# Optimization experiments

Measured on AMD Instinct MI355X. Metric: run time of the kernel, lower is better.

## Reference

```python
import jax, jax.numpy as jnp
import numpy as np

B, N, FEAT, HID, H = 4, 2048, 512, 512, 8
HD = HID // H  # head_dim = 64


def rotate_half(x):
    # pairs along last dim: (x1, x2) -> (-x2, x1), interleaved
    x = x.reshape(*x.shape[:-1], -1, 2)
    x1, x2 = x[..., 0], x[..., 1]
    return jnp.stack((-x2, x1), axis=-1).reshape(*x.shape[:-2], -1)


def apply_rope(freqs, t):
    # freqs: [2, B, 1, N, HD] broadcasting over heads; t: [B, H, N, HD]
    return t * freqs[0] + rotate_half(t) * freqs[1]


def setup_inputs() -> dict:
    key = jax.random.key(0)
    ks = jax.random.split(key, 12)
    s = 0.02
    return {
        "x0": jax.random.normal(ks[0], (B, N, FEAT), jnp.float32),
        "x1": jax.random.normal(ks[1], (B, N, FEAT), jnp.float32),
        "encoding0": jax.random.normal(ks[2], (2, B, 1, N, HD), jnp.float32),
        "encoding1": jax.random.normal(ks[3], (2, B, 1, N, HD), jnp.float32),
        "Wqkv": jax.random.normal(ks[4], (FEAT, 3 * HID), jnp.float32) * s,
        "bqkv": jnp.zeros((3 * HID,), jnp.float32),
        "Wproj": jax.random.normal(ks[5], (HID, HID), jnp.float32) * s,
        "bproj": jnp.zeros((HID,), jnp.float32),
        "W1": jax.random.normal(ks[6], (FEAT + HID, 2 * FEAT), jnp.float32) * s,
        "b1": jnp.zeros((2 * FEAT,), jnp.float32),
        "ln_g": jnp.ones((2 * FEAT,), jnp.float32),
        "ln_b": jnp.zeros((2 * FEAT,), jnp.float32),
        "W2": jax.random.normal(ks[7], (2 * FEAT, FEAT), jnp.float32) * s,
        "b2": jnp.zeros((FEAT,), jnp.float32),
    }


def _block(x, enc, Wqkv, bqkv, Wproj, bproj, W1, b1, ln_g, ln_b, W2, b2):
    b, n, _ = x.shape
    qkv = x @ Wqkv + bqkv                                   # [B,N,3*HID]
    qkv = qkv.reshape(b, n, H, HD, 3).transpose(0, 2, 1, 3, 4)  # [B,H,N,HD,3]
    q, k, v = qkv[..., 0], qkv[..., 1], qkv[..., 2]
    q = apply_rope(enc, q)
    k = apply_rope(enc, k)
    scale = q.shape[-1] ** (-0.5)
    attn = jax.nn.softmax(jnp.einsum('bhid,bhjd->bhij', q, k) * scale, axis=-1)
    o = jnp.einsum('bhij,bhjd->bhid', attn, v)              # [B,H,N,HD]
    message = o.transpose(0, 2, 1, 3).reshape(b, n, HID) @ Wproj + bproj
    h = jnp.concatenate([x, message], axis=-1) @ W1 + b1    # [B,N,2*FEAT]
    mu = h.mean(-1, keepdims=True)
    var = ((h - mu) ** 2).mean(-1, keepdims=True)
    h = (h - mu) * jax.lax.rsqrt(var + 1e-5) * ln_g + ln_b
    return x + jax.nn.gelu(h, approximate=False) @ W2 + b2


def reference(x0, x1, encoding0, encoding1, Wqkv, bqkv, Wproj, bproj, W1, b1, ln_g, ln_b, W2, b2):
    p = (Wqkv, bqkv, Wproj, bproj, W1, b1, ln_g, ln_b, W2, b2)
    return (_block(x0, encoding0, *p), _block(x1, encoding1, *p))
```

## Files before the change

### kernel.cpp

```cpp
#include <hip/hip_runtime.h>
#include <hip/hip_bf16.h>

typedef __attribute__((ext_vector_type(8))) short   short8v;
typedef __attribute__((ext_vector_type(4))) short   short4v;
typedef __attribute__((ext_vector_type(8))) __bf16  bf16x8;
typedef __attribute__((ext_vector_type(4))) __bf16  bf16x4;
typedef __attribute__((ext_vector_type(4))) float   f32x4;

constexpr int Nn = 2048;

#define GLOAD_LDS(src, dst) \
  __builtin_amdgcn_global_load_lds((__attribute__((address_space(1))) unsigned int*)(src), \
                                   (__attribute__((address_space(3))) unsigned int*)(dst), 16, 0, 0)

#if __has_builtin(__builtin_amdgcn_exp2f)
#define EXP2F(x) __builtin_amdgcn_exp2f(x)
#else
#define EXP2F(x) exp2f(x)
#endif

#if __has_builtin(__builtin_amdgcn_mfma_f32_16x16x16bf16_1k)
#define HAVE_MFMA16 1
#define MFMA16(a, b, c) __builtin_amdgcn_mfma_f32_16x16x16bf16_1k(a, b, c, 0, 0, 0)
#else
#define HAVE_MFMA16 0
#endif

__device__ __forceinline__ unsigned pack_bf16(float lo, float hi) {
  union { __bf16 h[2]; unsigned u; } t;
  t.h[0] = (__bf16)lo; t.h[1] = (__bf16)hi;
  return t.u;
}

template<int AMODE, int BMODE, int EPI>
__global__ __launch_bounds__(256)
void gemm_mfma(const __bf16* __restrict__ A, const __bf16* __restrict__ A2,
               const __bf16* __restrict__ BT, const __bf16* __restrict__ BT2,
               const float* __restrict__ bias,
               const float* __restrict__ resid0, const float* __restrict__ resid1,
               float* __restrict__ Cf, __bf16* __restrict__ Cb, __bf16* __restrict__ Vt,
               int lda, int ldb, int ldb2, int ldc, int K1, int K)
{
  __shared__ __align__(16) __bf16 As[3][4096];
  __shared__ __align__(16) __bf16 Bs[3][4096];
  const int tid = threadIdx.x;
  const int w = tid >> 6, l = tid & 63;
  const int wr = w >> 1, wc = w & 1;
  const int lr = l & 15, lg = l >> 4;
  const int row0 = blockIdx.x * 128, col0 = blockIdx.y * 128;

  f32x4 acc[4][4];
#pragma unroll
  for (int i = 0; i < 4; ++i)
#pragma unroll
    for (int j = 0; j < 4; ++j) acc[i][j] = (f32x4){0.f, 0.f, 0.f, 0.f};

  const int srow = l >> 2;
  const int skk  = (l & 3) * 8;

  auto stage = [&](int k0, int b) {
#pragma unroll
    for (int s = w; s < 8; s += 4) {
      const int m = s * 16 + srow;
      const __bf16* src;
      if constexpr (AMODE == 0) {
        src = A + (size_t)(row0 + m) * lda + k0 + skk;
      } else {
        const int gk = k0 + skk;
        src = (gk < K1) ? A  + (size_t)(row0 + m) * lda + gk
                        : A2 + (size_t)(row0 + m) * lda + (gk - K1);
      }
      GLOAD_LDS(src, &As[b][s * 512]);
    }
#pragma unroll
    for (int s = w; s < 8; s += 4) {
      const int n = s * 16 + srow;
      const __bf16* src;
      if constexpr (BMODE == 0) {
        src = BT + (size_t)(col0 + n) * ldb + k0 + skk;
      } else {
        const int gk = k0 + skk;
        src = (gk < K1) ? BT  + (size_t)(col0 + n) * ldb + gk
                        : BT2 + (size_t)(col0 + n) * ldb2 + (gk - K1);
      }
      GLOAD_LDS(src, &Bs[b][s * 512]);
    }
  };

  const int nt = K >> 5;
  stage(0, 0);
  if (nt > 1) stage(32, 1);
  asm volatile("s_waitcnt vmcnt(4)" ::: "memory");
  __builtin_amdgcn_sched_barrier(0);

  for (int t = 0; t < nt; ++t) {
    const int p = t % 3;
    __builtin_amdgcn_s_barrier();
    __builtin_amdgcn_sched_barrier(0);
    if (t + 2 < nt) stage((t + 2) * 32, (t + 2) % 3);
    bf16x8 af[4], bfv[4];
#pragma unroll
    for (int mi = 0; mi < 4; ++mi)
      af[mi] = *(const bf16x8*)&As[p][(wr * 64 + mi * 16 + lr) * 32 + lg * 8];
#pragma unroll
    for (int ni = 0; ni < 4; ++ni)
      bfv[ni] = *(const bf16x8*)&Bs[p][(wc * 64 + ni * 16 + lr) * 32 + lg * 8];
    __builtin_amdgcn_s_setprio(1);
#pragma unroll
    for (int mi = 0; mi < 4; ++mi)
#pragma unroll
      for (int ni = 0; ni < 4; ++ni)
        acc[mi][ni] = __builtin_amdgcn_mfma_f32_16x16x32_bf16(af[mi], bfv[ni], acc[mi][ni], 0, 0, 0);
    __builtin_amdgcn_s_setprio(0);
    if (t + 1 < nt) {
      if (t + 2 < nt) asm volatile("s_waitcnt vmcnt(4)" ::: "memory");
      else            asm volatile("s_waitcnt vmcnt(0)" ::: "memory");
    }
    __builtin_amdgcn_sched_barrier(0);
  }

  if constexpr (EPI == 4) {
    if (col0 >= 1024) {
      const int b2 = row0 >> 11;
#pragma unroll
      for (int mi = 0; mi < 4; ++mi)
#pragma unroll
        for (int ni = 0; ni < 4; ++ni) {
          const int col = col0 + wc * 64 + ni * 16 + lr;
          const int sec = col - 1024, h = sec >> 6, d = sec & 63;
          const int n0 = (row0 + wr * 64 + mi * 16 + lg * 4) & 2047;
          union { __bf16 h4[4]; short4 s4; } u;
#pragma unroll
          for (int r = 0; r < 4; ++r) u.h4[r] = (__bf16)(acc[mi][ni][r] + bias[col]);
          *(short4*)&Vt[(size_t)(b2 * 8 + h) * 131072 + (size_t)d * 2048 + n0] = u.s4;
        }
    } else {
      constexpr float SCQ = 0.125f * 1.44269504089f;
      const float* e = (row0 < 8192) ? resid0 : resid1;
#pragma unroll
      for (int mi = 0; mi < 4; ++mi)
#pragma unroll
        for (int ni = 0; ni < 4; ++ni) {
          const int col = col0 + wc * 64 + ni * 16 + lr;
          const int d = col & 63;
          const float sgn = (col & 1) ? 1.f : -1.f;
          const float scq = (col < 512) ? SCQ : 1.f;
#pragma unroll
          for (int r = 0; r < 4; ++r) {
            const int row = row0 + wr * 64 + mi * 16 + lg * 4 + r;
            const long bn = row & 8191;
            const float f0 = e[bn * 64 + d];
            const float f1 = e[524288 + bn * 64 + d];
            const float vb = acc[mi][ni][r] + bias[col];
            const float pb = __shfl_xor(vb, 1, 64);
            Cb[(size_t)row * 1024 + col] = (__bf16)((vb * f0 + sgn * pb * f1) * scq);
          }
        }
    }
    return;
  }

#pragma unroll
  for (int mi = 0; mi < 4; ++mi)
#pragma unroll
    for (int ni = 0; ni < 4; ++ni) {
      const int col = col0 + wc * 64 + ni * 16 + lr;
#pragma unroll
      for (int r = 0; r < 4; ++r) {
        const int row = row0 + wr * 64 + mi * 16 + lg * 4 + r;
        const float v = acc[mi][ni][r];
        if constexpr (EPI == 1) {
          Cb[(size_t)row * ldc + col] = (__bf16)(v + bias[col]);
        } else if constexpr (EPI == 3) {
          Cb[(size_t)row * ldc + col] = (__bf16)v;
        } else {
          const float* rp = (row < 8192) ? resid0 : resid1;
          Cf[(size_t)row * ldc + col] = v + bias[col] + rp[(size_t)(row & 8191) * ldc + col];
        }
      }
    }
}

__global__ __launch_bounds__(256, 2)
void fa_k(const __bf16* __restrict__ QK, const __bf16* __restrict__ Vg,
          __bf16* __restrict__ Ob)
{
  constexpr float FIXM = 8.f;
  __shared__ __align__(16) __bf16 Ks[3][4096];
  __shared__ __align__(16) __bf16 Vs[3][4096];
  const int tid = threadIdx.x;
  const int w = tid >> 6, l = tid & 63;
  const int lr = l & 15, lg = l >> 4;
  const int bid = blockIdx.x;
  const int qi = (bid >> 3) & 15;
  const int bh = (bid & 7) * 8 + (bid >> 7);
  const int b2 = bh >> 3, h = bh & 7;
  const __bf16* Qp = QK + (size_t)b2 * 2048 * 1024 + h * 64;
  const __bf16* Kp = Qp + 512;
  const __bf16* Vp = Vg + (size_t)bh * 131072;
  const int q0 = qi * 128 + w * 32;

  bf16x8 qf[2][2];
#pragma unroll
  for (int nf = 0; nf < 2; ++nf)
#pragma unroll
    for (int kk = 0; kk < 2; ++kk)
      qf[nf][kk] = *(const bf16x8*)&Qp[(size_t)(q0 + nf * 16 + lr) * 1024 + kk * 32 + lg * 8];

  f32x4 oacc[4][2];
#pragma unroll
  for (int i = 0; i < 4; ++i)
#pragma unroll
    for (int j = 0; j < 2; ++j) oacc[i][j] = (f32x4){0.f, 0.f, 0.f, 0.f};
  float rs[2] = {0.f, 0.f};

#if !HAVE_MFMA16
  const int Sa = (lg & 1) * 32 + lr, Sb2x = Sa + 16;
  const bool hi = (lg >> 1) & 1;
#endif

  auto stage = [&](int kv0, int b) {
#pragma unroll
    for (int i = 0; i < 2; ++i) {
      const int s = w + 4 * i;
      const int g = s * 64 + l, r = g >> 3, c = g & 7;
      GLOAD_LDS(Kp + (size_t)(kv0 + r) * 1024 + ((c ^ (r & 7)) * 8), &Ks[b][s * 512]);
      GLOAD_LDS(Vp + (size_t)r * 2048 + kv0 + ((c ^ (r & 7)) * 8), &Vs[b][s * 512]);
    }
  };

  stage(0, 0);
  stage(64, 1);
  asm volatile("s_waitcnt vmcnt(4)" ::: "memory");
  __builtin_amdgcn_sched_barrier(0);

  for (int t = 0; t < 32; ++t) {
    const int p = t % 3;
    __builtin_amdgcn_s_barrier();
    __builtin_amdgcn_sched_barrier(0);
    if (t + 2 < 32) stage((t + 2) * 64, (t + 2) % 3);

    f32x4 sacc[4][2];
#pragma unroll
    for (int i = 0; i < 4; ++i)
#pragma unroll
      for (int j = 0; j < 2; ++j) sacc[i][j] = (f32x4){0.f, 0.f, 0.f, 0.f};
#pragma unroll
    for (int kk = 0; kk < 2; ++kk) {
      bf16x8 ka[4];
#pragma unroll
      for (int mf = 0; mf < 4; ++mf)
        ka[mf] = *(const bf16x8*)&Ks[p][(mf * 16 + lr) * 64 + (((kk * 4 + lg) ^ (lr & 7)) * 8)];
      __builtin_amdgcn_s_setprio(1);
#pragma unroll
      for (int mf = 0; mf < 4; ++mf)
#pragma unroll
        for (int nf = 0; nf < 2; ++nf)
          sacc[mf][nf] = __builtin_amdgcn_mfma_f32_16x16x32_bf16(ka[mf], qf[nf][kk], sacc[mf][nf], 0, 0, 0);
      __builtin_amdgcn_s_setprio(0);
    }

    unsigned pkk[4][2][2];
#pragma unroll
    for (int nf = 0; nf < 2; ++nf) {
#pragma unroll
      for (int mf = 0; mf < 4; ++mf) {
        const float p0 = EXP2F(sacc[mf][nf][0] - FIXM);
        const float p1 = EXP2F(sacc[mf][nf][1] - FIXM);
        const float p2 = EXP2F(sacc[mf][nf][2] - FIXM);
        const float p3 = EXP2F(sacc[mf][nf][3] - FIXM);
        rs[nf] += (p0 + p1) + (p2 + p3);
        pkk[mf][nf][0] = pack_bf16(p0, p1);
        pkk[mf][nf][1] = pack_bf16(p2, p3);
      }
    }

#if HAVE_MFMA16
#pragma unroll
    for (int ks = 0; ks < 4; ++ks) {
      bf16x4 va[4];
#pragma unroll
      for (int mo = 0; mo < 4; ++mo) {
        const int g = (ks * 2 + (lg >> 1)) ^ (lr & 7);
        va[mo] = *(const bf16x4*)&Vs[p][(mo * 16 + lr) * 64 + g * 8 + (lg & 1) * 4];
      }
      __builtin_amdgcn_s_setprio(1);
#pragma unroll
      for (int mo = 0; mo < 4; ++mo)
#pragma unroll
        for (int nf = 0; nf < 2; ++nf)
          oacc[mo][nf] = MFMA16(__builtin_bit_cast(short4v, va[mo]),
                                __builtin_bit_cast(short4v, pkk[ks][nf]),
                                oacc[mo][nf]);
      __builtin_amdgcn_s_setprio(0);
    }
#else
#pragma unroll
    for (int kf = 0; kf < 2; ++kf) {
      bf16x8 va[4];
#pragma unroll
      for (int mo = 0; mo < 4; ++mo) {
        const int g = ((kf * 4 + lg) ^ (lr & 7));
        va[mo] = *(const bf16x8*)&Vs[p][(mo * 16 + lr) * 64 + g * 8];
      }
      bf16x8 bfr[2];
#pragma unroll
      for (int nf = 0; nf < 2; ++nf) {
        const unsigned s0 = hi ? pkk[kf * 2 + 1][nf][0] : pkk[kf * 2][nf][0];
        const unsigned s1 = hi ? pkk[kf * 2 + 1][nf][1] : pkk[kf * 2][nf][1];
        union { unsigned u[4]; bf16x8 v; } ub;
        ub.u[0] = (unsigned)__shfl((int)s0, Sa, 64);
        ub.u[1] = (unsigned)__shfl((int)s1, Sa, 64);
        ub.u[2] = (unsigned)__shfl((int)s0, Sb2x, 64);
        ub.u[3] = (unsigned)__shfl((int)s1, Sb2x, 64);
        bfr[nf] = ub.v;
      }
      __builtin_amdgcn_s_setprio(1);
#pragma unroll
      for (int mo = 0; mo < 4; ++mo)
#pragma unroll
        for (int nf = 0; nf < 2; ++nf)
          oacc[mo][nf] = __builtin_amdgcn_mfma_f32_16x16x32_bf16(va[mo], bfr[nf], oacc[mo][nf], 0, 0, 0);
      __builtin_amdgcn_s_setprio(0);
    }
#endif
    if (t < 31) {
      if (t + 2 < 32) asm volatile("s_waitcnt vmcnt(4)" ::: "memory");
      else            asm volatile("s_waitcnt vmcnt(0)" ::: "memory");
    }
    __builtin_amdgcn_sched_barrier(0);
  }

#pragma unroll
  for (int nf = 0; nf < 2; ++nf) {
    float ls = rs[nf];
    ls += __shfl_xor(ls, 16, 64);
    ls += __shfl_xor(ls, 32, 64);
    const float inv = 1.f / ls;
    const long row = (long)b2 * 2048 + q0 + nf * 16 + lr;
#pragma unroll
    for (int mo = 0; mo < 4; ++mo) {
      union { __bf16 h4[4]; short4 s4; } u;
#pragma unroll
      for (int r = 0; r < 4; ++r) u.h4[r] = (__bf16)(oacc[mo][nf][r] * inv);
      *(short4*)&Ob[row * 512 + h * 64 + mo * 16 + lg * 4] = u.s4;
    }
  }
}

__global__ __launch_bounds__(256)
void conv_f32_bf16_k(const float* __restrict__ s, __bf16* __restrict__ d)
{
  const long i = ((long)blockIdx.x * 256 + threadIdx.x) * 4;
  const float4 v = *(const float4*)&s[i];
  union { __bf16 h[4]; short4 sv; } u;
  u.h[0] = (__bf16)v.x; u.h[1] = (__bf16)v.y; u.h[2] = (__bf16)v.z; u.h[3] = (__bf16)v.w;
  *(short4*)&d[i] = u.sv;
}

__global__ __launch_bounds__(256)
void conv2_k(const float* __restrict__ x0, const float* __restrict__ x1,
             __bf16* __restrict__ d)
{
  const int bid = blockIdx.x;
  const float* s = (bid < 4096) ? x0 : x1;
  __bf16* dd = d + ((bid < 4096) ? 0 : 4194304);
  const long i = ((long)(bid & 4095) * 256 + threadIdx.x) * 4;
  const float4 v = *(const float4*)&s[i];
  union { __bf16 h[4]; short4 sv; } u;
  u.h[0] = (__bf16)v.x; u.h[1] = (__bf16)v.y; u.h[2] = (__bf16)v.z; u.h[3] = (__bf16)v.w;
  *(short4*)&dd[i] = u.sv;
}

__global__ __launch_bounds__(256)
void prep_wt_k(const float* __restrict__ Wqkv, const float* __restrict__ W1,
               const float* __restrict__ W2,
               __bf16* __restrict__ WqkvT, __bf16* __restrict__ W1T,
               __bf16* __restrict__ W2T)
{
  const int bid = blockIdx.x;
  const float* W; __bf16* WT; int K, N, bx, by; bool perm = false;
  if (bid < 768)       { W = Wqkv; WT = WqkvT; K = 512;  N = 1536; bx = bid % 48;          by = bid / 48;          perm = true; }
  else if (bid < 1792) { W = W1;   WT = W1T;   K = 1024; N = 1024; bx = (bid - 768) % 32;  by = (bid - 768) / 32; }
  else                 { W = W2;   WT = W2T;   K = 1024; N = 512;  bx = (bid - 1792) % 16; by = (bid - 1792) / 16; }
  __shared__ float t[32][33];
  const int n0 = bx * 32, k0 = by * 32;
  const int tx = threadIdx.x & 31, ty = threadIdx.x >> 5;
  for (int i = ty; i < 32; i += 8)
    t[i][tx] = W[(size_t)(k0 + i) * N + n0 + tx];
  __syncthreads();
  for (int i = ty; i < 32; i += 8) {
    int drow = n0 + i;
    if (perm) {
      const int h = drow / 192, rem = drow % 192;
      drow = (rem % 3) * 512 + h * 64 + rem / 3;
    }
    WT[(size_t)drow * K + k0 + tx] = (__bf16)t[tx][i];
  }
}

__global__ void bperm_k(const float* __restrict__ b, float* __restrict__ bp)
{
  const int i = blockIdx.x * 256 + threadIdx.x;
  if (i < 1536) {
    const int h = i / 192, rem = i % 192;
    bp[(rem % 3) * 512 + h * 64 + rem / 3] = b[i];
  }
}

__global__ __launch_bounds__(256)
void bfuse_k(const float* __restrict__ b1, const float* __restrict__ bproj,
             const float* __restrict__ W1, float* __restrict__ b1f)
{
  const int n = blockIdx.x * 256 + threadIdx.x;
  float s = b1[n];
  for (int m = 0; m < 512; ++m)
    s += bproj[m] * W1[(size_t)(512 + m) * 1024 + n];
  b1f[n] = s;
}

__global__ __launch_bounds__(256)
void ln_gelu_k(__bf16* __restrict__ Hb, const float* __restrict__ g,
               const float* __restrict__ be)
{
  __bf16* row = Hb + (size_t)blockIdx.x * 1024;
  const int tid = threadIdx.x;
  __shared__ float rs_[256], rq_[256];
  union { __bf16 h[4]; short4 sv; } u;
  u.sv = *(const short4*)&row[tid * 4];
  float v[4];
  float s = 0.f, sq = 0.f;
#pragma unroll
  for (int i = 0; i < 4; ++i) {
    v[i] = (float)u.h[i];
    s += v[i]; sq += v[i] * v[i];
  }
  rs_[tid] = s; rq_[tid] = sq; __syncthreads();
  for (int st = 128; st > 0; st >>= 1) {
    if (tid < st) { rs_[tid] += rs_[tid + st]; rq_[tid] += rq_[tid + st]; }
    __syncthreads();
  }
  const float mu = rs_[0] * (1.f / 1024.f);
  const float var = rq_[0] * (1.f / 1024.f) - mu * mu;
  const float rstd = rsqrtf(var + 1e-5f);
#pragma unroll
  for (int i = 0; i < 4; ++i) {
    const int c = tid * 4 + i;
    const float y = (v[i] - mu) * rstd * g[c] + be[c];
    u.h[i] = (__bf16)(0.5f * y * (1.f + erff(y * 0.70710678118f)));
  }
  *(short4*)&row[tid * 4] = u.sv;
}

extern "C" void kernel_launch(void* const* d_in, const int* in_sizes, int n_in,
                              void* d_out, int out_size, void* d_ws, size_t ws_size,
                              hipStream_t stream)
{
  const float* x0   = (const float*)d_in[0];
  const float* x1   = (const float*)d_in[1];
  const float* enc0 = (const float*)d_in[2];
  const float* enc1 = (const float*)d_in[3];
  const float* Wqkv  = (const float*)d_in[4];
  const float* bqkv  = (const float*)d_in[5];
  const float* Wproj = (const float*)d_in[6];
  const float* bproj = (const float*)d_in[7];
  const float* W1    = (const float*)d_in[8];
  const float* b1    = (const float*)d_in[9];
  const float* ln_g  = (const float*)d_in[10];
  const float* ln_b  = (const float*)d_in[11];
  const float* W2    = (const float*)d_in[12];
  const float* b2    = (const float*)d_in[13];

  __bf16* wsb = (__bf16*)d_ws;
  __bf16* xb      = wsb;
  __bf16* WqkvT   = wsb + 8388608;
  __bf16* Wproj_b = wsb + 9175040;
  __bf16* W1T     = wsb + 9437184;
  __bf16* W2T     = wsb + 10485760;
  float*  bqkvp   = (float*)(wsb + 11010048);
  __bf16* qkvb    = wsb + 11013120;
  __bf16* Vt      = wsb + 27790336;
  __bf16* Ob      = wsb + 36178944;
  __bf16* WfT     = wsb + 44567552;
  float*  b1f     = (float*)(wsb + 45091840);
  __bf16* hb      = qkvb;

  prep_wt_k<<<2304, 256, 0, stream>>>(Wqkv, W1, W2, WqkvT, W1T, W2T);
  bperm_k<<<6, 256, 0, stream>>>(bqkv, bqkvp);
  conv_f32_bf16_k<<<256, 256, 0, stream>>>(Wproj, Wproj_b);
  gemm_mfma<0, 0, 3><<<dim3(8, 4), 256, 0, stream>>>(
      W1T + 512, nullptr, Wproj_b, nullptr, nullptr, nullptr, nullptr,
      nullptr, WfT, nullptr, 1024, 512, 0, 512, 0, 512);
  bfuse_k<<<4, 256, 0, stream>>>(b1, bproj, W1, b1f);

  conv2_k<<<8192, 256, 0, stream>>>(x0, x1, xb);

  gemm_mfma<0, 0, 4><<<dim3(128, 12), 256, 0, stream>>>(
      xb, nullptr, WqkvT, nullptr, bqkvp, enc0, enc1, nullptr, qkvb, Vt,
      512, 512, 0, 1024, 0, 512);
  fa_k<<<1024, 256, 0, stream>>>(qkvb, Vt, Ob);
  gemm_mfma<1, 1, 1><<<dim3(128, 8), 256, 0, stream>>>(
      xb, Ob, W1T, WfT, b1f, nullptr, nullptr, nullptr, hb, nullptr,
      512, 1024, 512, 1024, 512, 1024);
  ln_gelu_k<<<16384, 256, 0, stream>>>(hb, ln_g, ln_b);
  gemm_mfma<0, 0, 2><<<dim3(128, 4), 256, 0, stream>>>(
      hb, nullptr, W2T, nullptr, b2, x0, x1, (float*)d_out, nullptr, nullptr,
      1024, 1024, 0, 512, 0, 1024);
}
```

Measured before the change: 320.4 us.

## Enlarge flash-attention query tile, merge prep kernels, use wave-per-row LayerNorm

```diff
diff --git a/kernel.cpp b/kernel.cpp
--- a/kernel.cpp
+++ b/kernel.cpp
@@ -192,27 +192,27 @@
   const int w = tid >> 6, l = tid & 63;
   const int lr = l & 15, lg = l >> 4;
   const int bid = blockIdx.x;
-  const int qi = (bid >> 3) & 15;
-  const int bh = (bid & 7) * 8 + (bid >> 7);
+  const int qi = (bid >> 3) & 7;
+  const int bh = (bid & 7) * 8 + (bid >> 6);
   const int b2 = bh >> 3, h = bh & 7;
   const __bf16* Qp = QK + (size_t)b2 * 2048 * 1024 + h * 64;
   const __bf16* Kp = Qp + 512;
   const __bf16* Vp = Vg + (size_t)bh * 131072;
-  const int q0 = qi * 128 + w * 32;
-
-  bf16x8 qf[2][2];
-#pragma unroll
-  for (int nf = 0; nf < 2; ++nf)
+  const int q0 = qi * 256 + w * 64;
+
+  bf16x8 qf[4][2];
+#pragma unroll
+  for (int nf = 0; nf < 4; ++nf)
 #pragma unroll
     for (int kk = 0; kk < 2; ++kk)
       qf[nf][kk] = *(const bf16x8*)&Qp[(size_t)(q0 + nf * 16 + lr) * 1024 + kk * 32 + lg * 8];
 
-  f32x4 oacc[4][2];
+  f32x4 oacc[4][4];
 #pragma unroll
   for (int i = 0; i < 4; ++i)
 #pragma unroll
-    for (int j = 0; j < 2; ++j) oacc[i][j] = (f32x4){0.f, 0.f, 0.f, 0.f};
-  float rs[2] = {0.f, 0.f};
+    for (int j = 0; j < 4; ++j) oacc[i][j] = (f32x4){0.f, 0.f, 0.f, 0.f};
+  float rs[4] = {0.f, 0.f, 0.f, 0.f};
 
 #if !HAVE_MFMA16
   const int Sa = (lg & 1) * 32 + lr, Sb2x = Sa + 16;
@@ -240,11 +240,11 @@
     __builtin_amdgcn_sched_barrier(0);
     if (t + 2 < 32) stage((t + 2) * 64, (t + 2) % 3);
 
-    f32x4 sacc[4][2];
+    f32x4 sacc[4][4];
 #pragma unroll
     for (int i = 0; i < 4; ++i)
 #pragma unroll
-      for (int j = 0; j < 2; ++j) sacc[i][j] = (f32x4){0.f, 0.f, 0.f, 0.f};
+      for (int j = 0; j < 4; ++j) sacc[i][j] = (f32x4){0.f, 0.f, 0.f, 0.f};
 #pragma unroll
     for (int kk = 0; kk < 2; ++kk) {
       bf16x8 ka[4];
@@ -255,14 +255,14 @@
 #pragma unroll
       for (int mf = 0; mf < 4; ++mf)
 #pragma unroll
-        for (int nf = 0; nf < 2; ++nf)
+        for (int nf = 0; nf < 4; ++nf)
           sacc[mf][nf] = __builtin_amdgcn_mfma_f32_16x16x32_bf16(ka[mf], qf[nf][kk], sacc[mf][nf], 0, 0, 0);
       __builtin_amdgcn_s_setprio(0);
     }
 
-    unsigned pkk[4][2][2];
-#pragma unroll
-    for (int nf = 0; nf < 2; ++nf) {
+    unsigned pkk[4][4][2];
+#pragma unroll
+    for (int nf = 0; nf < 4; ++nf) {
 #pragma unroll
       for (int mf = 0; mf < 4; ++mf) {
         const float p0 = EXP2F(sacc[mf][nf][0] - FIXM);
@@ -288,7 +288,7 @@
 #pragma unroll
       for (int mo = 0; mo < 4; ++mo)
 #pragma unroll
-        for (int nf = 0; nf < 2; ++nf)
+        for (int nf = 0; nf < 4; ++nf)
           oacc[mo][nf] = MFMA16(__builtin_bit_cast(short4v, va[mo]),
                                 __builtin_bit_cast(short4v, pkk[ks][nf]),
                                 oacc[mo][nf]);
@@ -303,9 +303,9 @@
         const int g = ((kf * 4 + lg) ^ (lr & 7));
         va[mo] = *(const bf16x8*)&Vs[p][(mo * 16 + lr) * 64 + g * 8];
       }
-      bf16x8 bfr[2];
-#pragma unroll
-      for (int nf = 0; nf < 2; ++nf) {
+      bf16x8 bfr[4];
+#pragma unroll
+      for (int nf = 0; nf < 4; ++nf) {
         const unsigned s0 = hi ? pkk[kf * 2 + 1][nf][0] : pkk[kf * 2][nf][0];
         const unsigned s1 = hi ? pkk[kf * 2 + 1][nf][1] : pkk[kf * 2][nf][1];
         union { unsigned u[4]; bf16x8 v; } ub;
@@ -319,7 +319,7 @@
 #pragma unroll
       for (int mo = 0; mo < 4; ++mo)
 #pragma unroll
-        for (int nf = 0; nf < 2; ++nf)
+        for (int nf = 0; nf < 4; ++nf)
           oacc[mo][nf] = __builtin_amdgcn_mfma_f32_16x16x32_bf16(va[mo], bfr[nf], oacc[mo][nf], 0, 0, 0);
       __builtin_amdgcn_s_setprio(0);
     }
@@ -332,7 +332,7 @@
   }
 
 #pragma unroll
-  for (int nf = 0; nf < 2; ++nf) {
+  for (int nf = 0; nf < 4; ++nf) {
     float ls = rs[nf];
     ls += __shfl_xor(ls, 16, 64);
     ls += __shfl_xor(ls, 32, 64);
@@ -349,107 +349,99 @@
 }
 
 __global__ __launch_bounds__(256)
-void conv_f32_bf16_k(const float* __restrict__ s, __bf16* __restrict__ d)
-{
-  const long i = ((long)blockIdx.x * 256 + threadIdx.x) * 4;
-  const float4 v = *(const float4*)&s[i];
-  union { __bf16 h[4]; short4 sv; } u;
-  u.h[0] = (__bf16)v.x; u.h[1] = (__bf16)v.y; u.h[2] = (__bf16)v.z; u.h[3] = (__bf16)v.w;
-  *(short4*)&d[i] = u.sv;
-}
-
-__global__ __launch_bounds__(256)
-void conv2_k(const float* __restrict__ x0, const float* __restrict__ x1,
-             __bf16* __restrict__ d)
+void prep_all_k(const float* __restrict__ x0, const float* __restrict__ x1,
+                const float* __restrict__ Wqkv, const float* __restrict__ W1,
+                const float* __restrict__ W2, const float* __restrict__ Wproj,
+                const float* __restrict__ bqkv, const float* __restrict__ b1,
+                const float* __restrict__ bproj,
+                __bf16* __restrict__ xb, __bf16* __restrict__ WqkvT,
+                __bf16* __restrict__ W1T, __bf16* __restrict__ W2T,
+                __bf16* __restrict__ Wproj_b, float* __restrict__ bqkvp,
+                float* __restrict__ b1f)
 {
   const int bid = blockIdx.x;
-  const float* s = (bid < 4096) ? x0 : x1;
-  __bf16* dd = d + ((bid < 4096) ? 0 : 4194304);
-  const long i = ((long)(bid & 4095) * 256 + threadIdx.x) * 4;
-  const float4 v = *(const float4*)&s[i];
-  union { __bf16 h[4]; short4 sv; } u;
-  u.h[0] = (__bf16)v.x; u.h[1] = (__bf16)v.y; u.h[2] = (__bf16)v.z; u.h[3] = (__bf16)v.w;
-  *(short4*)&dd[i] = u.sv;
-}
-
-__global__ __launch_bounds__(256)
-void prep_wt_k(const float* __restrict__ Wqkv, const float* __restrict__ W1,
-               const float* __restrict__ W2,
-               __bf16* __restrict__ WqkvT, __bf16* __restrict__ W1T,
-               __bf16* __restrict__ W2T)
-{
-  const int bid = blockIdx.x;
-  const float* W; __bf16* WT; int K, N, bx, by; bool perm = false;
-  if (bid < 768)       { W = Wqkv; WT = WqkvT; K = 512;  N = 1536; bx = bid % 48;          by = bid / 48;          perm = true; }
-  else if (bid < 1792) { W = W1;   WT = W1T;   K = 1024; N = 1024; bx = (bid - 768) % 32;  by = (bid - 768) / 32; }
-  else                 { W = W2;   WT = W2T;   K = 1024; N = 512;  bx = (bid - 1792) % 16; by = (bid - 1792) / 16; }
-  __shared__ float t[32][33];
-  const int n0 = bx * 32, k0 = by * 32;
-  const int tx = threadIdx.x & 31, ty = threadIdx.x >> 5;
-  for (int i = ty; i < 32; i += 8)
-    t[i][tx] = W[(size_t)(k0 + i) * N + n0 + tx];
-  __syncthreads();
-  for (int i = ty; i < 32; i += 8) {
-    int drow = n0 + i;
-    if (perm) {
-      const int h = drow / 192, rem = drow % 192;
-      drow = (rem % 3) * 512 + h * 64 + rem / 3;
-    }
-    WT[(size_t)drow * K + k0 + tx] = (__bf16)t[tx][i];
-  }
-}
-
-__global__ void bperm_k(const float* __restrict__ b, float* __restrict__ bp)
-{
-  const int i = blockIdx.x * 256 + threadIdx.x;
-  if (i < 1536) {
-    const int h = i / 192, rem = i % 192;
-    bp[(rem % 3) * 512 + h * 64 + rem / 3] = b[i];
-  }
-}
-
-__global__ __launch_bounds__(256)
-void bfuse_k(const float* __restrict__ b1, const float* __restrict__ bproj,
-             const float* __restrict__ W1, float* __restrict__ b1f)
-{
-  const int n = blockIdx.x * 256 + threadIdx.x;
-  float s = b1[n];
-  for (int m = 0; m < 512; ++m)
-    s += bproj[m] * W1[(size_t)(512 + m) * 1024 + n];
-  b1f[n] = s;
+  const int tid = threadIdx.x;
+  if (bid < 8192) {
+    const float* s = (bid < 4096) ? x0 : x1;
+    __bf16* dd = xb + ((bid < 4096) ? 0 : 4194304);
+    const long i = ((long)(bid & 4095) * 256 + tid) * 4;
+    const float4 v = *(const float4*)&s[i];
+    union { __bf16 h[4]; short4 sv; } u;
+    u.h[0] = (__bf16)v.x; u.h[1] = (__bf16)v.y; u.h[2] = (__bf16)v.z; u.h[3] = (__bf16)v.w;
+    *(short4*)&dd[i] = u.sv;
+  } else if (bid < 10496) {
+    const int b = bid - 8192;
+    const float* W; __bf16* WT; int K, N, bx, by; bool perm = false;
+    if (b < 768)       { W = Wqkv; WT = WqkvT; K = 512;  N = 1536; bx = b % 48;         by = b / 48;         perm = true; }
+    else if (b < 1792) { W = W1;   WT = W1T;   K = 1024; N = 1024; bx = (b - 768) % 32; by = (b - 768) / 32; }
+    else               { W = W2;   WT = W2T;   K = 1024; N = 512;  bx = (b - 1792) % 16; by = (b - 1792) / 16; }
+    __shared__ float t[32][33];
+    const int n0 = bx * 32, k0 = by * 32;
+    const int tx = tid & 31, ty = tid >> 5;
+    for (int i = ty; i < 32; i += 8)
+      t[i][tx] = W[(size_t)(k0 + i) * N + n0 + tx];
+    __syncthreads();
+    for (int i = ty; i < 32; i += 8) {
+      int drow = n0 + i;
+      if (perm) {
+        const int hh = drow / 192, rem = drow % 192;
+        drow = (rem % 3) * 512 + hh * 64 + rem / 3;
+      }
+      WT[(size_t)drow * K + k0 + tx] = (__bf16)t[tx][i];
+    }
+  } else if (bid < 10752) {
+    const long i = ((long)(bid - 10496) * 256 + tid) * 4;
+    const float4 v = *(const float4*)&Wproj[i];
+    union { __bf16 h[4]; short4 sv; } u;
+    u.h[0] = (__bf16)v.x; u.h[1] = (__bf16)v.y; u.h[2] = (__bf16)v.z; u.h[3] = (__bf16)v.w;
+    *(short4*)&Wproj_b[i] = u.sv;
+  } else if (bid < 10758) {
+    const int i = (bid - 10752) * 256 + tid;
+    if (i < 1536) {
+      const int hh = i / 192, rem = i % 192;
+      bqkvp[(rem % 3) * 512 + hh * 64 + rem / 3] = bqkv[i];
+    }
+  } else {
+    const int n = (bid - 10758) * 256 + tid;
+    float s = b1[n];
+    for (int m = 0; m < 512; ++m)
+      s += bproj[m] * W1[(size_t)(512 + m) * 1024 + n];
+    b1f[n] = s;
+  }
 }
 
 __global__ __launch_bounds__(256)
 void ln_gelu_k(__bf16* __restrict__ Hb, const float* __restrict__ g,
                const float* __restrict__ be)
 {
-  __bf16* row = Hb + (size_t)blockIdx.x * 1024;
-  const int tid = threadIdx.x;
-  __shared__ float rs_[256], rq_[256];
-  union { __bf16 h[4]; short4 sv; } u;
-  u.sv = *(const short4*)&row[tid * 4];
-  float v[4];
+  const int w = threadIdx.x >> 6, l = threadIdx.x & 63;
+  __bf16* rp = Hb + ((size_t)blockIdx.x * 4 + w) * 1024;
+  union { __bf16 h[8]; short8v sv; } u0, u1;
+  u0.sv = *(const short8v*)&rp[l * 16];
+  u1.sv = *(const short8v*)&rp[l * 16 + 8];
+  float v[16];
   float s = 0.f, sq = 0.f;
 #pragma unroll
-  for (int i = 0; i < 4; ++i) {
-    v[i] = (float)u.h[i];
-    s += v[i]; sq += v[i] * v[i];
-  }
-  rs_[tid] = s; rq_[tid] = sq; __syncthreads();
-  for (int st = 128; st > 0; st >>= 1) {
-    if (tid < st) { rs_[tid] += rs_[tid + st]; rq_[tid] += rq_[tid + st]; }
-    __syncthreads();
-  }
-  const float mu = rs_[0] * (1.f / 1024.f);
-  const float var = rq_[0] * (1.f / 1024.f) - mu * mu;
+  for (int i = 0; i < 8; ++i) { v[i] = (float)u0.h[i]; v[8 + i] = (float)u1.h[i]; }
+#pragma unroll
+  for (int i = 0; i < 16; ++i) { s += v[i]; sq += v[i] * v[i]; }
+#pragma unroll
+  for (int d = 32; d > 0; d >>= 1) {
+    s  += __shfl_xor(s, d, 64);
+    sq += __shfl_xor(sq, d, 64);
+  }
+  const float mu = s * (1.f / 1024.f);
+  const float var = sq * (1.f / 1024.f) - mu * mu;
   const float rstd = rsqrtf(var + 1e-5f);
 #pragma unroll
-  for (int i = 0; i < 4; ++i) {
-    const int c = tid * 4 + i;
+  for (int i = 0; i < 16; ++i) {
+    const int c = l * 16 + i;
     const float y = (v[i] - mu) * rstd * g[c] + be[c];
-    u.h[i] = (__bf16)(0.5f * y * (1.f + erff(y * 0.70710678118f)));
-  }
-  *(short4*)&row[tid * 4] = u.sv;
+    const float o = 0.5f * y * (1.f + erff(y * 0.70710678118f));
+    if (i < 8) u0.h[i] = (__bf16)o; else u1.h[i - 8] = (__bf16)o;
+  }
+  *(short8v*)&rp[l * 16] = u0.sv;
+  *(short8v*)&rp[l * 16 + 8] = u1.sv;
 }
 
 extern "C" void kernel_launch(void* const* d_in, const int* in_sizes, int n_in,
@@ -485,24 +477,21 @@
   float*  b1f     = (float*)(wsb + 45091840);
   __bf16* hb      = qkvb;
 
-  prep_wt_k<<<2304, 256, 0, stream>>>(Wqkv, W1, W2, WqkvT, W1T, W2T);
-  bperm_k<<<6, 256, 0, stream>>>(bqkv, bqkvp);
-  conv_f32_bf16_k<<<256, 256, 0, stream>>>(Wproj, Wproj_b);
+  prep_all_k<<<10762, 256, 0, stream>>>(x0, x1, Wqkv, W1, W2, Wproj,
+                                        bqkv, b1, bproj,
+                                        xb, WqkvT, W1T, W2T, Wproj_b, bqkvp, b1f);
   gemm_mfma<0, 0, 3><<<dim3(8, 4), 256, 0, stream>>>(
       W1T + 512, nullptr, Wproj_b, nullptr, nullptr, nullptr, nullptr,
       nullptr, WfT, nullptr, 1024, 512, 0, 512, 0, 512);
-  bfuse_k<<<4, 256, 0, stream>>>(b1, bproj, W1, b1f);
-
-  conv2_k<<<8192, 256, 0, stream>>>(x0, x1, xb);
 
   gemm_mfma<0, 0, 4><<<dim3(128, 12), 256, 0, stream>>>(
       xb, nullptr, WqkvT, nullptr, bqkvp, enc0, enc1, nullptr, qkvb, Vt,
       512, 512, 0, 1024, 0, 512);
-  fa_k<<<1024, 256, 0, stream>>>(qkvb, Vt, Ob);
+  fa_k<<<512, 256, 0, stream>>>(qkvb, Vt, Ob);
   gemm_mfma<1, 1, 1><<<dim3(128, 8), 256, 0, stream>>>(
       xb, Ob, W1T, WfT, b1f, nullptr, nullptr, nullptr, hb, nullptr,
       512, 1024, 512, 1024, 512, 1024);
-  ln_gelu_k<<<16384, 256, 0, stream>>>(hb, ln_g, ln_b);
+  ln_gelu_k<<<4096, 256, 0, stream>>>(hb, ln_g, ln_b);
   gemm_mfma<0, 0, 2><<<dim3(128, 4), 256, 0, stream>>>(
       hb, nullptr, W2T, nullptr, b2, x0, x1, (float*)d_out, nullptr, nullptr,
       1024, 1024, 0, 512, 0, 1024);
```

Measured after the change: 333.9 us. 1.04x slower.
